# Optimization experiments

Measured on AMD Instinct MI355X. Metric: run time of the kernel, lower is better.

## Reference

```python
import jax, jax.numpy as jnp
import numpy as np

DIM = 128
WS = 16      # window size
HALO = 8     # halo size
HEADS = 8
HD = DIM // HEADS
HIDDEN = DIM * 4
EPS = 1e-5


def _ln(x, w, b):
    # LayerNorm over last (channel) axis, like nn.LayerNorm(channels)
    mu = jnp.mean(x, axis=-1, keepdims=True)
    var = jnp.var(x, axis=-1, keepdims=True)
    return (x - mu) * jax.lax.rsqrt(var + EPS) * w + b


def _halo_windows(t):
    # t: [B,H,W,C] -> overlapping halo windows [B,nH,nW,K*K,C]
    B, H, W, C = t.shape
    K = WS + 2 * HALO
    nH, nW = H // WS, W // WS
    tp = jnp.pad(t, ((0, 0), (HALO, HALO), (HALO, HALO), (0, 0)))
    ih = jnp.arange(nH)[:, None] * WS + jnp.arange(K)[None, :]  # [nH,K]
    iw = jnp.arange(nW)[:, None] * WS + jnp.arange(K)[None, :]  # [nW,K]
    t1 = tp[:, ih]            # [B,nH,K,W+2h,C]
    t2 = t1[:, :, :, iw]      # [B,nH,K,nW,K,C]
    return t2.transpose(0, 1, 3, 2, 4, 5).reshape(B, nH, nW, K * K, C)


def _query_windows(t):
    # t: [B,H,W,C] -> non-overlapping windows [B,nH,nW,WS*WS,C]
    B, H, W, C = t.shape
    nH, nW = H // WS, W // WS
    return (t.reshape(B, nH, WS, nW, WS, C)
             .transpose(0, 1, 3, 2, 4, 5)
             .reshape(B, nH, nW, WS * WS, C))


def _halo_attention(h, qkv_w, qkv_b, proj_w, proj_b):
    # h: [B,H,W,C] channels-last
    B, H, W, C = h.shape
    nH, nW = H // WS, W // WS
    K = WS + 2 * HALO
    qkv = h @ qkv_w.T + qkv_b                       # [B,H,W,3C]
    q, k, v = jnp.split(qkv, 3, axis=-1)
    qw = _query_windows(q).reshape(B, nH, nW, WS * WS, HEADS, HD)
    kw = _halo_windows(k).reshape(B, nH, nW, K * K, HEADS, HD)
    vw = _halo_windows(v).reshape(B, nH, nW, K * K, HEADS, HD)
    scale = HD ** -0.5
    scores = jnp.einsum('bxyqhd,bxykhd->bxyhqk', qw * scale, kw)
    attn = jax.nn.softmax(scores, axis=-1)
    out = jnp.einsum('bxyhqk,bxykhd->bxyqhd', attn, vw)
    out = (out.reshape(B, nH, nW, WS, WS, C)
              .transpose(0, 1, 3, 2, 4, 5)
              .reshape(B, H, W, C))
    return out @ proj_w.T + proj_b


def setup_inputs() -> dict:
    key = jax.random.key(0)
    ks = jax.random.split(key, 12)
    s = lambda k, shape, fan: jax.random.normal(k, shape, jnp.float32) * (fan ** -0.5)
    return {
        'x': jax.random.normal(ks[0], (1, DIM, 128, 128), jnp.float32),
        'ln1_w': jnp.ones((DIM,), jnp.float32),
        'ln1_b': jnp.zeros((DIM,), jnp.float32),
        'qkv_w': s(ks[1], (3 * DIM, DIM), DIM),
        'qkv_b': jnp.zeros((3 * DIM,), jnp.float32),
        'proj_w': s(ks[2], (DIM, DIM), DIM),
        'proj_b': jnp.zeros((DIM,), jnp.float32),
        'ln2_w': jnp.ones((DIM,), jnp.float32),
        'ln2_b': jnp.zeros((DIM,), jnp.float32),
        'fc1_w': s(ks[3], (HIDDEN, DIM), DIM),
        'fc1_b': jnp.zeros((HIDDEN,), jnp.float32),
        'fc2_w': s(ks[4], (DIM, HIDDEN), HIDDEN),
        'fc2_b': jnp.zeros((DIM,), jnp.float32),
    }


def reference(x, ln1_w, ln1_b, qkv_w, qkv_b, proj_w, proj_b,
              ln2_w, ln2_b, fc1_w, fc1_b, fc2_w, fc2_b):
    # x: [B,C,H,W]
    xh = x.transpose(0, 2, 3, 1)                    # BHWC
    h = _ln(xh, ln1_w, ln1_b)
    attn_out = _halo_attention(h, qkv_w, qkv_b, proj_w, proj_b)
    xh = xh + attn_out                              # residual 1
    h2 = _ln(xh, ln2_w, ln2_b)
    m = jax.nn.gelu(h2 @ fc1_w.T + fc1_b, approximate=False) @ fc2_w.T + fc2_b
    xh = xh + m                                     # residual 2 (dropout=0)
    return xh.transpose(0, 3, 1, 2)                 # back to NCHW
```

## Files before the change

kernel.cpp:

```cpp
#include <hip/hip_runtime.h>
#include <hip/hip_bf16.h>


typedef __attribute__((ext_vector_type(8))) short bf16x8;
typedef __attribute__((ext_vector_type(4))) float f32x4;
typedef __attribute__((ext_vector_type(4))) unsigned int u32x4;

#define MFMA16(a, b, c) __builtin_amdgcn_mfma_f32_16x16x32_bf16((a), (b), (c), 0, 0, 0)

__device__ __forceinline__ float u2f(unsigned short u) {
  unsigned int x = ((unsigned int)u) << 16;
  return __builtin_bit_cast(float, x);
}
__device__ __forceinline__ unsigned short f2u(float f) {
  unsigned int x = __builtin_bit_cast(unsigned int, f);
  x += 0x7FFFu + ((x >> 16) & 1u);
  return (unsigned short)(x >> 16);
}
__device__ __forceinline__ unsigned int cvt_pk_bf16(float lo, float hi) {
  unsigned int r;
  asm("v_cvt_pk_bf16_f32 %0, %1, %2" : "=v"(r) : "v"(lo), "v"(hi));
  return r;
}

#define QSCALE 0.36067376022224085f

#define O_XHT 0ull
#define O_H1  (8ull << 20)
#define O_QB  (12ull << 20)
#define O_XH1 (16ull << 20)
#define O_KP  (24ull << 20)
#define O_VPT (O_KP + 5308416ull)
#define O_M1  O_KP
#define O_WB  (O_KP + (16ull << 20))
#define PADT  20736

__global__ __launch_bounds__(256) void setup_kernel(
    const float* __restrict__ a, const float* __restrict__ b,
    const float* __restrict__ c, const float* __restrict__ d,
    unsigned short* __restrict__ wb,
    unsigned short* __restrict__ kp, unsigned short* __restrict__ vpt) {
  const int bx = blockIdx.x, tid = threadIdx.x;
  if (bx < 192) {
    const int i = (bx * 256 + tid) * 4;
    const float* s; int lo;
    if (i < 49152)       { s = a; lo = 0; }
    else if (i < 65536)  { s = b; lo = 49152; }
    else if (i < 131072) { s = c; lo = 65536; }
    else                 { s = d; lo = 131072; }
    const float4 v = *(const float4*)(s + (i - lo));
    ushort4 o;
    o.x = f2u(v.x); o.y = f2u(v.y); o.z = f2u(v.z); o.w = f2u(v.w);
    *(ushort4*)(wb + i) = o;
  } else if (bx < 209) {
    const int idx = (bx - 192) * 256 + tid;
    if (idx >= 4352) return;
    int r, cc;
    if (idx < 2304) {
      const int rr = idx / 144;
      r = (rr < 8) ? rr : rr + 128;
      cc = idx - rr * 144;
    } else {
      const int i2 = idx - 2304;
      r = 8 + (i2 >> 4);
      const int c2 = i2 & 15;
      cc = (c2 < 8) ? c2 : c2 + 128;
    }
    const size_t off = ((size_t)r * 144 + cc) * 128;
    const u32x4 z = {};
#pragma unroll
    for (int k = 0; k < 16; k++) *(u32x4*)(kp + off + k * 8) = z;
  } else {
    const int ch = bx - 209;
    unsigned short* base = vpt + (size_t)ch * PADT;
    const u32x4 z = {};
    if (tid < 144) {
      *(u32x4*)(base + tid * 8) = z;
      *(u32x4*)(base + 19584 + tid * 8) = z;
    }
    const int hr = tid >> 1, side = tid & 1;
    *(u32x4*)(base + (hr + 8) * 144 + side * 136) = z;
  }
}

__global__ __launch_bounds__(256) void ln1_kernel(
    const float* __restrict__ x,
    const float* __restrict__ lw, const float* __restrict__ lb,
    float* __restrict__ xh_t, unsigned short* __restrict__ h1) {
  __shared__ float ld[128][33];
  const int t0 = blockIdx.x * 32;
  const int tid = threadIdx.x;
  {
    const int c = tid >> 1, th = (tid & 1) * 16;
    const float* src = x + (size_t)c * 16384 + t0 + th;
#pragma unroll
    for (int i = 0; i < 4; i++) {
      const float4 v = *(const float4*)(src + i * 4);
      ld[c][th + i * 4]     = v.x;
      ld[c][th + i * 4 + 1] = v.y;
      ld[c][th + i * 4 + 2] = v.z;
      ld[c][th + i * 4 + 3] = v.w;
    }
  }
  __syncthreads();
  const int t = tid >> 3, cp = (tid & 7) * 16;
  float vals[16];
  float s = 0.f, q = 0.f;
#pragma unroll
  for (int i = 0; i < 16; i++) {
    const float v = ld[cp + i][t];
    vals[i] = v;
    s += v; q += v * v;
  }
  s += __shfl_xor(s, 1); q += __shfl_xor(q, 1);
  s += __shfl_xor(s, 2); q += __shfl_xor(q, 2);
  s += __shfl_xor(s, 4); q += __shfl_xor(q, 4);
  const float mu = s * 0.0078125f;
  const float rs = rsqrtf(q * 0.0078125f - mu * mu + 1e-5f);
  float* xrow = xh_t + (size_t)(t0 + t) * 128 + cp;
#pragma unroll
  for (int i = 0; i < 4; i++)
    *(float4*)(xrow + i * 4) =
        float4{vals[4*i], vals[4*i+1], vals[4*i+2], vals[4*i+3]};
  unsigned int pk[8];
#pragma unroll
  for (int k = 0; k < 8; k++) {
    const float y0 = (vals[2*k]   - mu) * rs * lw[cp + 2*k]   + lb[cp + 2*k];
    const float y1 = (vals[2*k+1] - mu) * rs * lw[cp + 2*k+1] + lb[cp + 2*k+1];
    pk[k] = cvt_pk_bf16(y0, y1);
  }
  unsigned int* hrow = (unsigned int*)(h1 + (size_t)(t0 + t) * 128 + cp);
  *(u32x4*)(hrow)     = u32x4{pk[0], pk[1], pk[2], pk[3]};
  *(u32x4*)(hrow + 4) = u32x4{pk[4], pk[5], pk[6], pk[7]};
}

enum { EPI_QKV = 0, EPI_GELU = 2, EPI_FC2 = 3 };

template <int EPI, int K>
__global__ __launch_bounds__(64) void gemm_kernel(
    const unsigned short* __restrict__ A,
    const unsigned short* __restrict__ B,
    const float* __restrict__ bias,
    void* __restrict__ o0, void* __restrict__ o1, void* __restrict__ o2,
    const void* __restrict__ aux) {
  const int tid = threadIdx.x;
  const int lr = tid & 15, lg = tid >> 4;
  const int mB = blockIdx.x * 64, nB = blockIdx.y * 64;
  f32x4 acc[4][4] = {};
  const unsigned short* Ab = A + (size_t)(mB + lr) * K + lg * 8;
  const unsigned short* Bb = B + (size_t)(nB + lr) * K + lg * 8;
  for (int k = 0; k < K; k += 32) {
    bf16x8 a[4], b[4];
#pragma unroll
    for (int i = 0; i < 4; i++) {
      a[i] = *(const bf16x8*)(Ab + (size_t)i * 16 * K + k);
      b[i] = *(const bf16x8*)(Bb + (size_t)i * 16 * K + k);
    }
#pragma unroll
    for (int i = 0; i < 4; i++)
#pragma unroll
      for (int j = 0; j < 4; j++)
        acc[i][j] = MFMA16(a[i], b[j], acc[i][j]);
  }

  if constexpr (EPI == EPI_FC2) {
    __shared__ float tb[64][68];
#pragma unroll
    for (int j = 0; j < 4; j++) {
      const int jl = j * 16 + lr;
      const float bv = bias[nB + jl];
#pragma unroll
      for (int i = 0; i < 4; i++)
#pragma unroll
        for (int r = 0; r < 4; r++) {
          const int il = i * 16 + lg * 4 + r;
          tb[jl][il] = acc[i][j][r] + bv +
                       ((const float*)aux)[(size_t)(mB + il) * 128 + (nB + jl)];
        }
    }
    __syncthreads();
    float* op = (float*)o0 + (size_t)(nB + tid) * 16384 + mB;
#pragma unroll
    for (int kk = 0; kk < 16; kk++)
      *(float4*)(op + kk * 4) = *(const float4*)&tb[tid][kk * 4];
  } else if constexpr (EPI == EPI_QKV) {
    if (nB < 256) {
#pragma unroll
      for (int j = 0; j < 4; j++) {
        const int jj = nB + j * 16 + lr;
        const float bv = bias[jj];
#pragma unroll
        for (int i = 0; i < 4; i++)
#pragma unroll
          for (int r = 0; r < 4; r++) {
            const int ii = mB + i * 16 + lg * 4 + r;
            const float v = acc[i][j][r] + bv;
            if (jj < 128) {
              ((unsigned short*)o0)[(size_t)ii * 128 + jj] = f2u(v * QSCALE);
            } else {
              const int gh = ii >> 7, gw = ii & 127;
              const size_t prow = (size_t)(gh + 8) * 144 + (gw + 8);
              ((unsigned short*)o1)[prow * 128 + (jj - 128)] = f2u(v);
            }
          }
      }
    } else {
      __shared__ __align__(16) unsigned short tbv[64][72];
#pragma unroll
      for (int j = 0; j < 4; j++) {
        const int jl = j * 16 + lr;
        const float bv = bias[nB + jl];
#pragma unroll
        for (int i = 0; i < 4; i++)
#pragma unroll
          for (int r = 0; r < 4; r++) {
            const int il = i * 16 + lg * 4 + r;
            tbv[jl][il] = f2u(acc[i][j][r] + bv);
          }
      }
      __syncthreads();
      const int gh = mB >> 7, gw0 = mB & 127;
      const size_t prow0 = (size_t)(gh + 8) * 144 + gw0 + 8;
      unsigned short* dst =
          (unsigned short*)o2 + (size_t)(nB - 256 + tid) * PADT + prow0;
#pragma unroll
      for (int t8 = 0; t8 < 8; t8++)
        *(u32x4*)(dst + t8 * 8) = *(const u32x4*)&tbv[tid][t8 * 8];
    }
  } else {
#pragma unroll
    for (int j = 0; j < 4; j++) {
      const int jj = nB + j * 16 + lr;
      const float bv = bias[jj];
#pragma unroll
      for (int i = 0; i < 4; i++)
#pragma unroll
        for (int r = 0; r < 4; r++) {
          const int ii = mB + i * 16 + lg * 4 + r;
          const float v = acc[i][j][r] + bv;
          const float y = 0.7978845608f * (v + 0.044715f * v * v * v);
          const float E = __builtin_amdgcn_exp2f(y * 2.8853900818f);
          const float g = v - v * __builtin_amdgcn_rcpf(E + 1.0f);
          ((unsigned short*)o0)[(size_t)ii * 512 + jj] = f2u(g);
        }
    }
  }
}

__global__ __launch_bounds__(256) void projln2_kernel(
    const unsigned short* __restrict__ A,
    const unsigned short* __restrict__ B,
    const float* __restrict__ bias,
    const float* __restrict__ xh_t,
    const float* __restrict__ lw, const float* __restrict__ lb,
    float* __restrict__ xh1, unsigned short* __restrict__ h2) {
  __shared__ float sred[4][16][2];
  const int tid = threadIdx.x;
  const int w = tid >> 6, l = tid & 63;
  const int lr = l & 15, lg = l >> 4;
  const int mB = blockIdx.x * 16;
  const int n0 = w * 32;
  f32x4 acc[2] = {};
  const unsigned short* Ar = A + (size_t)(mB + lr) * 128 + lg * 8;
  const unsigned short* Br0 = B + (size_t)(n0 + lr) * 128 + lg * 8;
  const unsigned short* Br1 = Br0 + 16 * 128;
  for (int k = 0; k < 128; k += 32) {
    const bf16x8 a  = *(const bf16x8*)(Ar + k);
    const bf16x8 b0 = *(const bf16x8*)(Br0 + k);
    const bf16x8 b1 = *(const bf16x8*)(Br1 + k);
    acc[0] = MFMA16(a, b0, acc[0]);
    acc[1] = MFMA16(a, b1, acc[1]);
  }
  float vv[2][4];
#pragma unroll
  for (int j = 0; j < 2; j++) {
    const int jj = n0 + j * 16 + lr;
    const float bv = bias[jj];
#pragma unroll
    for (int r = 0; r < 4; r++) {
      const int ii = mB + lg * 4 + r;
      const float v = acc[j][r] + bv + xh_t[(size_t)ii * 128 + jj];
      xh1[(size_t)ii * 128 + jj] = v;
      vv[j][r] = v;
    }
  }
#pragma unroll
  for (int r = 0; r < 4; r++) {
    float s = vv[0][r] + vv[1][r];
    float q = vv[0][r] * vv[0][r] + vv[1][r] * vv[1][r];
    s += __shfl_xor(s, 1); q += __shfl_xor(q, 1);
    s += __shfl_xor(s, 2); q += __shfl_xor(q, 2);
    s += __shfl_xor(s, 4); q += __shfl_xor(q, 4);
    s += __shfl_xor(s, 8); q += __shfl_xor(q, 8);
    if (lr == 0) {
      sred[w][lg * 4 + r][0] = s;
      sred[w][lg * 4 + r][1] = q;
    }
  }
  __syncthreads();
#pragma unroll
  for (int r = 0; r < 4; r++) {
    const int tok = lg * 4 + r;
    const float s = sred[0][tok][0] + sred[1][tok][0] +
                    sred[2][tok][0] + sred[3][tok][0];
    const float q = sred[0][tok][1] + sred[1][tok][1] +
                    sred[2][tok][1] + sred[3][tok][1];
    const float mu = s * 0.0078125f;
    const float rs = rsqrtf(q * 0.0078125f - mu * mu + 1e-5f);
#pragma unroll
    for (int j = 0; j < 2; j++) {
      const int jj = n0 + j * 16 + lr;
      const float y = (vv[j][r] - mu) * rs * lw[jj] + lb[jj];
      h2[(size_t)(mB + tok) * 128 + jj] = f2u(y);
    }
  }
}

__global__ __launch_bounds__(256) void attn_kernel(
    const unsigned short* __restrict__ qb,
    const unsigned short* __restrict__ kp,
    const unsigned short* __restrict__ vpt,
    unsigned short* __restrict__ attnb) {
  __shared__ __align__(16) unsigned int pl[4][16][20];
  __shared__ __align__(16) unsigned short K_lds[32][32][16];
  const int bid = blockIdx.x;
  const int win = bid & 63;
  const int sub = bid >> 6;
  const int qh = sub & 1, head = sub >> 1;
  const int wy = win >> 3, wx = win & 7;
  const int tid = threadIdx.x;
  const int wv = tid >> 6, l = tid & 63;
  const int lr = l & 15, lg = l >> 4;

#pragma unroll
  for (int it = 0; it < 4; it++) {
    const int idx = it * 256 + tid;
    const int krr = idx >> 5, key = idx & 31;
    const unsigned short* src =
        kp + ((size_t)(wy * 16 + krr) * 144 + wx * 16 + key) * 128 + head * 16;
    *(u32x4*)&K_lds[krr][key][0] = *(const u32x4*)src;
    *(u32x4*)&K_lds[krr][key][8] = *(const u32x4*)(src + 8);
  }

  bf16x8 qf[2];
#pragma unroll
  for (int qt = 0; qt < 2; qt++) {
    bf16x8 t = {};
    if (lg < 2) {
      const int qi = qh * 128 + wv * 32 + qt * 16 + lr;
      const int gh = wy * 16 + (qi >> 4), gw = wx * 16 + (qi & 15);
      t = *(const bf16x8*)(qb + ((size_t)(gh * 128 + gw)) * 128 + head * 16 + lg * 8);
    }
    qf[qt] = t;
  }

  bf16x8 ones;
#pragma unroll
  for (int e = 0; e < 8; e++) ones[e] = (short)0x3F80;

  f32x4 acc[2] = {}, den[2] = {};
  unsigned int* wp = &pl[wv][lr][lg * 4];
  const unsigned int* rp = &pl[wv][lr][(lg & 1) * 8];
  const unsigned int psel = (lg >= 2) ? 0x07060302u : 0x05040100u;

  const unsigned short* vbase =
      vpt + (size_t)(head * 16 + lr) * PADT + (size_t)(wy * 16) * 144 + wx * 16 + lg * 8;

  __syncthreads();

  for (int kr = 0; kr < 32; kr++) {
    bf16x8 kf0 = {}, kf1 = {};
    if (lg < 2) {
      kf0 = *(const bf16x8*)&K_lds[kr][lr][lg * 8];
      kf1 = *(const bf16x8*)&K_lds[kr][16 + lr][lg * 8];
    }
    const bf16x8 vf = *(const bf16x8*)(vbase + kr * 144);
#pragma unroll
    for (int qt = 0; qt < 2; qt++) {
      f32x4 s0 = {}, s1 = {};
      s0 = MFMA16(kf0, qf[qt], s0);
      s1 = MFMA16(kf1, qf[qt], s1);
      unsigned int pk[4];
#pragma unroll
      for (int r = 0; r < 4; r++)
        pk[r] = cvt_pk_bf16(__builtin_amdgcn_exp2f(s0[r]),
                            __builtin_amdgcn_exp2f(s1[r]));
      *(u32x4*)wp = u32x4{pk[0], pk[1], pk[2], pk[3]};
      const u32x4 in0 = *(const u32x4*)(rp);
      const u32x4 in1 = *(const u32x4*)(rp + 4);
      u32x4 pa;
      pa[0] = __builtin_amdgcn_perm(in0[1], in0[0], psel);
      pa[1] = __builtin_amdgcn_perm(in0[3], in0[2], psel);
      pa[2] = __builtin_amdgcn_perm(in1[1], in1[0], psel);
      pa[3] = __builtin_amdgcn_perm(in1[3], in1[2], psel);
      const bf16x8 paf = __builtin_bit_cast(bf16x8, pa);
      acc[qt] = MFMA16(paf, vf, acc[qt]);
      den[qt] = MFMA16(paf, ones, den[qt]);
    }
  }

#pragma unroll
  for (int qt = 0; qt < 2; qt++)
#pragma unroll
    for (int r = 0; r < 4; r++) {
      const int q0 = qt * 16 + lg * 4 + r;
      const int qi2 = qh * 128 + wv * 32 + q0;
      const int gh2 = wy * 16 + (qi2 >> 4), gw2 = wx * 16 + (qi2 & 15);
      attnb[((size_t)(gh2 * 128 + gw2)) * 128 + head * 16 + lr] =
          f2u(acc[qt][r] * __builtin_amdgcn_rcpf(den[qt][r]));
    }
}

extern "C" void kernel_launch(void* const* d_in, const int* in_sizes, int n_in,
                              void* d_out, int out_size, void* d_ws, size_t ws_size,
                              hipStream_t stream) {
  const float* x      = (const float*)d_in[0];
  const float* ln1w   = (const float*)d_in[1];
  const float* ln1b   = (const float*)d_in[2];
  const float* qkv_w  = (const float*)d_in[3];
  const float* qkv_b  = (const float*)d_in[4];
  const float* proj_w = (const float*)d_in[5];
  const float* proj_b = (const float*)d_in[6];
  const float* ln2w   = (const float*)d_in[7];
  const float* ln2b   = (const float*)d_in[8];
  const float* fc1_w  = (const float*)d_in[9];
  const float* fc1_b  = (const float*)d_in[10];
  const float* fc2_w  = (const float*)d_in[11];
  const float* fc2_b  = (const float*)d_in[12];

  char* ws = (char*)d_ws;
  float*          xh_t = (float*)(ws + O_XHT);
  unsigned short* h1   = (unsigned short*)(ws + O_H1);
  unsigned short* qb   = (unsigned short*)(ws + O_QB);
  float*          xh1  = (float*)(ws + O_XH1);
  unsigned short* kp   = (unsigned short*)(ws + O_KP);
  unsigned short* vpt  = (unsigned short*)(ws + O_VPT);
  unsigned short* m1   = (unsigned short*)(ws + O_M1);
  unsigned short* wb   = (unsigned short*)(ws + O_WB);
  unsigned short* attnb = h1;
  unsigned short* h2    = qb;
  float* outp = (float*)d_out;

  unsigned short* qkv_wb  = wb;
  unsigned short* proj_wb = wb + 49152;
  unsigned short* fc1_wb  = wb + 65536;
  unsigned short* fc2_wb  = wb + 131072;

  setup_kernel<<<337, 256, 0, stream>>>(qkv_w, proj_w, fc1_w, fc2_w, wb, kp, vpt);
  ln1_kernel<<<512, 256, 0, stream>>>(x, ln1w, ln1b, xh_t, h1);
  gemm_kernel<EPI_QKV, 128><<<dim3(256, 6), 64, 0, stream>>>(
      h1, qkv_wb, qkv_b, qb, kp, vpt, nullptr);
  attn_kernel<<<1024, 256, 0, stream>>>(qb, kp, vpt, attnb);
  projln2_kernel<<<1024, 256, 0, stream>>>(
      attnb, proj_wb, proj_b, xh_t, ln2w, ln2b, xh1, h2);
  gemm_kernel<EPI_GELU, 128><<<dim3(256, 8), 64, 0, stream>>>(
      h2, fc1_wb, fc1_b, m1, nullptr, nullptr, nullptr);
  gemm_kernel<EPI_FC2, 512><<<dim3(256, 2), 64, 0, stream>>>(
      m1, fc2_wb, fc2_b, outp, nullptr, nullptr, xh1);
}
```

Measured before the change: 104.7 us.

## Fuse fc1+GELU and fc2+residual into one MLP kernel keeping hidden in LDS

Replaces the separate fc1/GELU GEMM and fc2/residual GEMM launches with a single mlp_kernel. Each block computes 64 tokens' 512-wide hidden activations, stores them as bf16 in shared memory, then runs fc2 from LDS and writes the transposed output. This removes the global round-trip of the 16384x512 hidden tensor and one launch. In exchange it uses about 65 KB of LDS per block and only 256 blocks, which lowers occupancy and parallelism. The QKV GEMM is split out of the old template into its own kernel with the same logic.

```diff
diff --git a/kernel.cpp b/kernel.cpp
--- a/kernel.cpp
+++ b/kernel.cpp
@@ -21,6 +21,11 @@
   unsigned int r;
   asm("v_cvt_pk_bf16_f32 %0, %1, %2" : "=v"(r) : "v"(lo), "v"(hi));
   return r;
+}
+__device__ __forceinline__ float gelu_f(float v) {
+  const float y = 0.7978845608f * (v + 0.044715f * v * v * v);
+  const float E = __builtin_amdgcn_exp2f(y * 2.8853900818f);
+  return v - v * __builtin_amdgcn_rcpf(E + 1.0f);
 }
 
 #define QSCALE 0.36067376022224085f
@@ -31,7 +36,6 @@
 #define O_XH1 (16ull << 20)
 #define O_KP  (24ull << 20)
 #define O_VPT (O_KP + 5308416ull)
-#define O_M1  O_KP
 #define O_WB  (O_KP + (16ull << 20))
 #define PADT  20736
 
@@ -134,27 +138,25 @@
   *(u32x4*)(hrow + 4) = u32x4{pk[4], pk[5], pk[6], pk[7]};
 }
 
-enum { EPI_QKV = 0, EPI_GELU = 2, EPI_FC2 = 3 };
-
-template <int EPI, int K>
-__global__ __launch_bounds__(64) void gemm_kernel(
+__global__ __launch_bounds__(64) void qkv_kernel(
     const unsigned short* __restrict__ A,
     const unsigned short* __restrict__ B,
     const float* __restrict__ bias,
-    void* __restrict__ o0, void* __restrict__ o1, void* __restrict__ o2,
-    const void* __restrict__ aux) {
+    unsigned short* __restrict__ qb,
+    unsigned short* __restrict__ kp,
+    unsigned short* __restrict__ vpt) {
   const int tid = threadIdx.x;
   const int lr = tid & 15, lg = tid >> 4;
   const int mB = blockIdx.x * 64, nB = blockIdx.y * 64;
   f32x4 acc[4][4] = {};
-  const unsigned short* Ab = A + (size_t)(mB + lr) * K + lg * 8;
-  const unsigned short* Bb = B + (size_t)(nB + lr) * K + lg * 8;
-  for (int k = 0; k < K; k += 32) {
+  const unsigned short* Ab = A + (size_t)(mB + lr) * 128 + lg * 8;
+  const unsigned short* Bb = B + (size_t)(nB + lr) * 128 + lg * 8;
+  for (int k = 0; k < 128; k += 32) {
     bf16x8 a[4], b[4];
 #pragma unroll
     for (int i = 0; i < 4; i++) {
-      a[i] = *(const bf16x8*)(Ab + (size_t)i * 16 * K + k);
-      b[i] = *(const bf16x8*)(Bb + (size_t)i * 16 * K + k);
+      a[i] = *(const bf16x8*)(Ab + (size_t)i * 16 * 128 + k);
+      b[i] = *(const bf16x8*)(Bb + (size_t)i * 16 * 128 + k);
     }
 #pragma unroll
     for (int i = 0; i < 4; i++)
@@ -163,8 +165,28 @@
         acc[i][j] = MFMA16(a[i], b[j], acc[i][j]);
   }
 
-  if constexpr (EPI == EPI_FC2) {
-    __shared__ float tb[64][68];
+  if (nB < 256) {
+#pragma unroll
+    for (int j = 0; j < 4; j++) {
+      const int jj = nB + j * 16 + lr;
+      const float bv = bias[jj];
+#pragma unroll
+      for (int i = 0; i < 4; i++)
+#pragma unroll
+        for (int r = 0; r < 4; r++) {
+          const int ii = mB + i * 16 + lg * 4 + r;
+          const float v = acc[i][j][r] + bv;
+          if (jj < 128) {
+            qb[(size_t)ii * 128 + jj] = f2u(v * QSCALE);
+          } else {
+            const int gh = ii >> 7, gw = ii & 127;
+            const size_t prow = (size_t)(gh + 8) * 144 + (gw + 8);
+            kp[prow * 128 + (jj - 128)] = f2u(v);
+          }
+        }
+    }
+  } else {
+    __shared__ __align__(16) unsigned short tbv[64][72];
 #pragma unroll
     for (int j = 0; j < 4; j++) {
       const int jl = j * 16 + lr;
@@ -174,76 +196,16 @@
 #pragma unroll
         for (int r = 0; r < 4; r++) {
           const int il = i * 16 + lg * 4 + r;
-          tb[jl][il] = acc[i][j][r] + bv +
-                       ((const float*)aux)[(size_t)(mB + il) * 128 + (nB + jl)];
+          tbv[jl][il] = f2u(acc[i][j][r] + bv);
         }
     }
     __syncthreads();
-    float* op = (float*)o0 + (size_t)(nB + tid) * 16384 + mB;
-#pragma unroll
-    for (int kk = 0; kk < 16; kk++)
-      *(float4*)(op + kk * 4) = *(const float4*)&tb[tid][kk * 4];
-  } else if constexpr (EPI == EPI_QKV) {
-    if (nB < 256) {
-#pragma unroll
-      for (int j = 0; j < 4; j++) {
-        const int jj = nB + j * 16 + lr;
-        const float bv = bias[jj];
-#pragma unroll
-        for (int i = 0; i < 4; i++)
-#pragma unroll
-          for (int r = 0; r < 4; r++) {
-            const int ii = mB + i * 16 + lg * 4 + r;
-            const float v = acc[i][j][r] + bv;
-            if (jj < 128) {
-              ((unsigned short*)o0)[(size_t)ii * 128 + jj] = f2u(v * QSCALE);
-            } else {
-              const int gh = ii >> 7, gw = ii & 127;
-              const size_t prow = (size_t)(gh + 8) * 144 + (gw + 8);
-              ((unsigned short*)o1)[prow * 128 + (jj - 128)] = f2u(v);
-            }
-          }
-      }
-    } else {
-      __shared__ __align__(16) unsigned short tbv[64][72];
-#pragma unroll
-      for (int j = 0; j < 4; j++) {
-        const int jl = j * 16 + lr;
-        const float bv = bias[nB + jl];
-#pragma unroll
-        for (int i = 0; i < 4; i++)
-#pragma unroll
-          for (int r = 0; r < 4; r++) {
-            const int il = i * 16 + lg * 4 + r;
-            tbv[jl][il] = f2u(acc[i][j][r] + bv);
-          }
-      }
-      __syncthreads();
-      const int gh = mB >> 7, gw0 = mB & 127;
-      const size_t prow0 = (size_t)(gh + 8) * 144 + gw0 + 8;
-      unsigned short* dst =
-          (unsigned short*)o2 + (size_t)(nB - 256 + tid) * PADT + prow0;
-#pragma unroll
-      for (int t8 = 0; t8 < 8; t8++)
-        *(u32x4*)(dst + t8 * 8) = *(const u32x4*)&tbv[tid][t8 * 8];
-    }
-  } else {
-#pragma unroll
-    for (int j = 0; j < 4; j++) {
-      const int jj = nB + j * 16 + lr;
-      const float bv = bias[jj];
-#pragma unroll
-      for (int i = 0; i < 4; i++)
-#pragma unroll
-        for (int r = 0; r < 4; r++) {
-          const int ii = mB + i * 16 + lg * 4 + r;
-          const float v = acc[i][j][r] + bv;
-          const float y = 0.7978845608f * (v + 0.044715f * v * v * v);
-          const float E = __builtin_amdgcn_exp2f(y * 2.8853900818f);
-          const float g = v - v * __builtin_amdgcn_rcpf(E + 1.0f);
-          ((unsigned short*)o0)[(size_t)ii * 512 + jj] = f2u(g);
-        }
-    }
+    const int gh = mB >> 7, gw0 = mB & 127;
+    const size_t prow0 = (size_t)(gh + 8) * 144 + gw0 + 8;
+    unsigned short* dst = vpt + (size_t)(nB - 256 + tid) * PADT + prow0;
+#pragma unroll
+    for (int t8 = 0; t8 < 8; t8++)
+      *(u32x4*)(dst + t8 * 8) = *(const u32x4*)&tbv[tid][t8 * 8];
   }
 }
 
@@ -316,6 +278,104 @@
   }
 }
 
+__global__ __launch_bounds__(256) void mlp_kernel(
+    const unsigned short* __restrict__ h2,
+    const unsigned short* __restrict__ fc1_wb,
+    const float* __restrict__ fc1_b,
+    const unsigned short* __restrict__ fc2_wb,
+    const float* __restrict__ fc2_b,
+    const float* __restrict__ xh1,
+    float* __restrict__ outp) {
+  __shared__ __align__(16) char smem[66560];
+  unsigned short (*m_lds)[520] = (unsigned short(*)[520])smem;
+  float (*tb)[68] = (float(*)[68])smem;
+
+  const int tid = threadIdx.x;
+  const int w = tid >> 6, l = tid & 63;
+  const int lr = l & 15, lg = l >> 4;
+  const int mB = blockIdx.x * 64;
+
+  {
+    f32x4 acc[8][4] = {};
+    const unsigned short* Ab = fc1_wb + (size_t)(w * 128 + lr) * 128 + lg * 8;
+    const unsigned short* Bb = h2 + (size_t)(mB + lr) * 128 + lg * 8;
+    for (int k = 0; k < 128; k += 32) {
+      bf16x8 a[8], b[4];
+#pragma unroll
+      for (int i = 0; i < 8; i++)
+        a[i] = *(const bf16x8*)(Ab + (size_t)i * 16 * 128 + k);
+#pragma unroll
+      for (int j = 0; j < 4; j++)
+        b[j] = *(const bf16x8*)(Bb + (size_t)j * 16 * 128 + k);
+#pragma unroll
+      for (int i = 0; i < 8; i++)
+#pragma unroll
+        for (int j = 0; j < 4; j++)
+          acc[i][j] = MFMA16(a[i], b[j], acc[i][j]);
+    }
+#pragma unroll
+    for (int i = 0; i < 8; i++) {
+      const int n0 = w * 128 + i * 16 + lg * 4;
+      const float4 b4 = *(const float4*)(fc1_b + n0);
+#pragma unroll
+      for (int j = 0; j < 4; j++) {
+        const int t = j * 16 + lr;
+        const float g0 = gelu_f(acc[i][j][0] + b4.x);
+        const float g1 = gelu_f(acc[i][j][1] + b4.y);
+        const float g2 = gelu_f(acc[i][j][2] + b4.z);
+        const float g3 = gelu_f(acc[i][j][3] + b4.w);
+        uint2 pk;
+        pk.x = cvt_pk_bf16(g0, g1);
+        pk.y = cvt_pk_bf16(g2, g3);
+        *(uint2*)&m_lds[t][n0] = pk;
+      }
+    }
+  }
+  __syncthreads();
+
+  f32x4 acc2[4][2] = {};
+  {
+    const unsigned short* Bb = fc2_wb + (size_t)(w * 32 + lr) * 512 + lg * 8;
+    for (int k = 0; k < 512; k += 32) {
+      bf16x8 a[4], b[2];
+#pragma unroll
+      for (int i = 0; i < 4; i++)
+        a[i] = *(const bf16x8*)&m_lds[i * 16 + lr][k + lg * 8];
+#pragma unroll
+      for (int j = 0; j < 2; j++)
+        b[j] = *(const bf16x8*)(Bb + (size_t)j * 16 * 512 + k);
+#pragma unroll
+      for (int i = 0; i < 4; i++)
+#pragma unroll
+        for (int j = 0; j < 2; j++)
+          acc2[i][j] = MFMA16(a[i], b[j], acc2[i][j]);
+    }
+  }
+  __syncthreads();
+
+#pragma unroll
+  for (int j = 0; j < 2; j++) {
+    const int jj = w * 32 + j * 16 + lr;
+    const float bv = fc2_b[jj];
+#pragma unroll
+    for (int i = 0; i < 4; i++)
+#pragma unroll
+      for (int r = 0; r < 4; r++) {
+        const int il = i * 16 + lg * 4 + r;
+        tb[jj][il] = acc2[i][j][r] + bv +
+                     xh1[(size_t)(mB + il) * 128 + jj];
+      }
+  }
+  __syncthreads();
+  {
+    const int c = tid >> 1, seg = (tid & 1) * 32;
+    float* op = outp + (size_t)c * 16384 + mB + seg;
+#pragma unroll
+    for (int q = 0; q < 8; q++)
+      *(float4*)(op + q * 4) = *(const float4*)&tb[c][seg + q * 4];
+  }
+}
+
 __global__ __launch_bounds__(256) void attn_kernel(
     const unsigned short* __restrict__ qb,
     const unsigned short* __restrict__ kp,
@@ -435,7 +495,6 @@
   float*          xh1  = (float*)(ws + O_XH1);
   unsigned short* kp   = (unsigned short*)(ws + O_KP);
   unsigned short* vpt  = (unsigned short*)(ws + O_VPT);
-  unsigned short* m1   = (unsigned short*)(ws + O_M1);
   unsigned short* wb   = (unsigned short*)(ws + O_WB);
   unsigned short* attnb = h1;
   unsigned short* h2    = qb;
@@ -448,13 +507,9 @@
 
   setup_kernel<<<337, 256, 0, stream>>>(qkv_w, proj_w, fc1_w, fc2_w, wb, kp, vpt);
   ln1_kernel<<<512, 256, 0, stream>>>(x, ln1w, ln1b, xh_t, h1);
-  gemm_kernel<EPI_QKV, 128><<<dim3(256, 6), 64, 0, stream>>>(
-      h1, qkv_wb, qkv_b, qb, kp, vpt, nullptr);
+  qkv_kernel<<<dim3(256, 6), 64, 0, stream>>>(h1, qkv_wb, qkv_b, qb, kp, vpt);
   attn_kernel<<<1024, 256, 0, stream>>>(qb, kp, vpt, attnb);
   projln2_kernel<<<1024, 256, 0, stream>>>(
       attnb, proj_wb, proj_b, xh_t, ln2w, ln2b, xh1, h2);
-  gemm_kernel<EPI_GELU, 128><<<dim3(256, 8), 64, 0, stream>>>(
-      h2, fc1_wb, fc1_b, m1, nullptr, nullptr, nullptr);
-  gemm_kernel<EPI_FC2, 512><<<dim3(256, 2), 64, 0, stream>>>(
-      m1, fc2_wb, fc2_b, outp, nullptr, nullptr, xh1);
-}
+  mlp_kernel<<<256, 256, 0, stream>>>(h2, fc1_wb, fc1_b, fc2_wb, fc2_b, xh1, outp);
+}
```

Result: faster. 96.61 us (-7.7%).
